# Optimization experiments

Hardware: AMD Instinct MI355X
Metric: run time of the kernel (lower is better)

The kernel has to match this reference:

```python
import jax, jax.numpy as jnp
import numpy as np

N = 10000        # nodes
E = 320000       # edges (avg degree 32)
H = 256          # num_hidden
NH = 8           # num_heads
NIN = 512        # num_in = 2*H


def _lin(key, out_f, in_f, scale=0.02):
    kw, kb = jax.random.split(key)
    W = jax.random.normal(kw, (out_f, in_f), jnp.float32) * scale
    b = jax.random.normal(kb, (out_f,), jnp.float32) * scale
    return W, b


def setup_inputs() -> dict:
    key = jax.random.key(0)
    ks = jax.random.split(key, 12)
    src_na = jax.random.normal(ks[0], (N, H), jnp.float32)
    dst_na = jax.random.normal(ks[1], (N, H), jnp.float32)
    ea = jax.random.normal(ks[2], (E, H), jnp.float32)
    edge_idx = jax.random.randint(ks[3], (2, E), 0, N, dtype=jnp.int32).astype(jnp.int64)
    # W_V: Linear(NIN,H) GELU Linear(H,H) GELU Linear(H,H)
    Wv1, bv1 = _lin(ks[4], H, NIN)
    Wv2, bv2 = _lin(ks[5], H, H)
    Wv3, bv3 = _lin(ks[6], H, H)
    # Bias: Linear(3H,H) ReLU Linear(H,H) ReLU Linear(H,NH)
    Wb1, bb1 = _lin(ks[7], H, 3 * H)
    Wb2, bb2 = _lin(ks[8], H, H)
    Wb3, bb3 = _lin(ks[9], NH, H)
    WO = jax.random.normal(ks[10], (H, H), jnp.float32) * 0.02  # no bias
    return dict(src_na=src_na, dst_na=dst_na, ea=ea, edge_idx=edge_idx,
                Wv1=Wv1, bv1=bv1, Wv2=Wv2, bv2=bv2, Wv3=Wv3, bv3=bv3,
                Wb1=Wb1, bb1=bb1, Wb2=Wb2, bb2=bb2, Wb3=Wb3, bb3=bb3, WO=WO)


def reference(src_na, dst_na, ea, edge_idx,
              Wv1, bv1, Wv2, bv2, Wv3, bv3,
              Wb1, bb1, Wb2, bb2, Wb3, bb3, WO):
    num_hidden = src_na.shape[-1]
    num_heads = Wb3.shape[0]
    d = num_hidden // num_heads
    n_nodes = dst_na.shape[0]

    dst_idx = edge_idx[0]
    src_idx = edge_idx[1]

    s = src_na[src_idx]          # [E,H] gather
    t = dst_na[dst_idx]          # [E,H] gather

    # Bias MLP -> per-edge, per-head logits
    h = jax.nn.relu(jnp.concatenate([s, ea, t], axis=-1) @ Wb1.T + bb1)
    h = jax.nn.relu(h @ Wb2.T + bb2)
    w = h @ Wb3.T + bb3                                  # [E,NH]
    logits = (w / np.sqrt(d)).reshape(-1, num_heads, 1)  # [E,NH,1]

    # Value MLP
    v = jax.nn.gelu(jnp.concatenate([s, ea], axis=-1) @ Wv1.T + bv1, approximate=False)
    v = jax.nn.gelu(v @ Wv2.T + bv2, approximate=False)
    V = (v @ Wv3.T + bv3).reshape(-1, num_heads, d)      # [E,NH,d]

    # scatter_softmax over edges grouped by destination node
    m = jax.ops.segment_max(logits, dst_idx, num_segments=n_nodes)   # [N,NH,1]
    ex = jnp.exp(logits - m[dst_idx])
    denom = jax.ops.segment_sum(ex, dst_idx, num_segments=n_nodes)   # [N,NH,1]
    attend = ex / denom[dst_idx]                                     # [E,NH,1]

    agg = jax.ops.segment_sum(attend * V, dst_idx, num_segments=n_nodes)  # [N,NH,d]
    out = agg.reshape(n_nodes, num_hidden) @ WO.T
    return out
```

## Files before the change

### kernel.cpp

```cpp
#include <hip/hip_runtime.h>
#include <hip/hip_bf16.h>
#include <cstdint>
#include <cstddef>

#define EN 320000
#define NN 10000

typedef __bf16 bf16_t;
typedef __bf16 bf16x8 __attribute__((ext_vector_type(8)));
typedef float f32x4 __attribute__((ext_vector_type(4)));
typedef unsigned short u16x8 __attribute__((ext_vector_type(8)));

__device__ __forceinline__ unsigned short f2b(float x) {
  bf16_t h = (bf16_t)x;
  return __builtin_bit_cast(unsigned short, h);
}
__device__ __forceinline__ float gelu_f(float x) {
  return 0.5f * x * (1.0f + erff(x * 0.70710678118654752f));
}
__device__ __forceinline__ void async_cp16(const void* gp, void* lp) {
  __builtin_amdgcn_global_load_lds((__attribute__((address_space(1))) void*)gp,
                                   (__attribute__((address_space(3))) void*)lp,
                                   16, 0, 0);
}

template <int AMODE, int EPI>
__global__ __launch_bounds__(256) void gemm_k(
    const void* __restrict__ Av, const bf16_t* __restrict__ W,
    const float* __restrict__ bias, void* __restrict__ Cv,
    int M, int K, int NOUT,
    const int* __restrict__ src32, const int* __restrict__ dst32,
    const float* __restrict__ projS, const float* __restrict__ projT,
    const float* __restrict__ bias2, bf16_t* __restrict__ C2) {
  __shared__ __align__(16) unsigned short As[128 * 32];
  __shared__ __align__(16) unsigned short Bs[128 * 32];
  const int tid = threadIdx.x;
  const int lane = tid & 63;
  const int wave = tid >> 6;
  const int wm = wave & 1, wn = wave >> 1;
  const int fr = lane & 15, kg = lane >> 4;
  const int rowBase = blockIdx.y * 128;
  const int colBase = blockIdx.x * 128;

  f32x4 acc[4][4] = {};

  const int nK = K >> 5;
  for (int kt = 0; kt < nK; ++kt) {
    const int k0 = kt << 5;
    if (kt) __syncthreads();
    if constexpr (AMODE == 0) {
      const bf16_t* A = (const bf16_t*)Av;
#pragma unroll
      for (int c = 0; c < 2; ++c) {
        int r = wave * 32 + c * 16 + (lane >> 2);
        int gr = rowBase + r;
        gr = (gr < M) ? gr : (M - 1);
        async_cp16(A + (size_t)gr * K + k0 + (lane & 3) * 8,
                   &As[(wave * 32 + c * 16) * 32]);
        int wr = colBase + wave * 32 + c * 16 + (lane >> 2);
        async_cp16(W + (size_t)wr * K + k0 + (lane & 3) * 8,
                   &Bs[(wave * 32 + c * 16) * 32]);
      }
    } else {
      const float* A = (const float*)Av;
      int r = tid >> 1, hh = tid & 1;
      int gr = rowBase + r;
      gr = (gr < M) ? gr : (M - 1);
      const float4* gp = (const float4*)(A + (size_t)gr * K + k0 + hh * 16);
      float4 x0 = gp[0], x1 = gp[1], x2 = gp[2], x3 = gp[3];
      u16x8 p0 = {f2b(x0.x), f2b(x0.y), f2b(x0.z), f2b(x0.w),
                  f2b(x1.x), f2b(x1.y), f2b(x1.z), f2b(x1.w)};
      u16x8 p1 = {f2b(x2.x), f2b(x2.y), f2b(x2.z), f2b(x2.w),
                  f2b(x3.x), f2b(x3.y), f2b(x3.z), f2b(x3.w)};
      *(u16x8*)&As[r * 32 + hh * 16] = p0;
      *(u16x8*)&As[r * 32 + hh * 16 + 8] = p1;
      const u16x8* wp = (const u16x8*)(W + (size_t)(colBase + r) * K + k0 + hh * 16);
      *(u16x8*)&Bs[r * 32 + hh * 16] = wp[0];
      *(u16x8*)&Bs[r * 32 + hh * 16 + 8] = wp[1];
    }
    __syncthreads();
    bf16x8 af[4], bw[4];
#pragma unroll
    for (int i = 0; i < 4; ++i)
      af[i] = *(const bf16x8*)&As[(wm * 64 + i * 16 + fr) * 32 + kg * 8];
#pragma unroll
    for (int i = 0; i < 4; ++i)
      bw[i] = *(const bf16x8*)&Bs[(wn * 64 + i * 16 + fr) * 32 + kg * 8];
#pragma unroll
    for (int mi = 0; mi < 4; ++mi)
#pragma unroll
      for (int ni = 0; ni < 4; ++ni)
        acc[mi][ni] = __builtin_amdgcn_mfma_f32_16x16x32_bf16(
            af[mi], bw[ni], acc[mi][ni], 0, 0, 0);
  }

  const int r0 = rowBase + wm * 64;
  const int c0 = colBase + wn * 64;
  if constexpr (EPI == 0) {
    float* C = (float*)Cv;
#pragma unroll
    for (int mi = 0; mi < 4; ++mi)
#pragma unroll
      for (int reg = 0; reg < 4; ++reg) {
        int row = r0 + mi * 16 + kg * 4 + reg;
        if (row < M) {
#pragma unroll
          for (int ni = 0; ni < 4; ++ni) {
            int col = c0 + ni * 16 + fr;
            C[(size_t)row * NOUT + col] = acc[mi][ni][reg];
          }
        }
      }
  } else if constexpr (EPI == 4) {
    bf16_t* C = (bf16_t*)Cv;
#pragma unroll
    for (int mi = 0; mi < 4; ++mi)
#pragma unroll
      for (int reg = 0; reg < 4; ++reg) {
        int e = r0 + mi * 16 + kg * 4 + reg;
        int si = src32[e], di = dst32[e];
#pragma unroll
        for (int ni = 0; ni < 4; ++ni) {
          int col = c0 + ni * 16 + fr;
          float v = acc[mi][ni][reg];
          if (col < 256) {
            v += bias[col] + projS[(size_t)si * 512 + col] + projT[(size_t)di * 256 + col];
            v = fmaxf(v, 0.f);
            C[(size_t)e * 256 + col] = (bf16_t)v;
          } else {
            int c2 = col - 256;
            v += bias2[c2] + projS[(size_t)si * 512 + col];
            v = gelu_f(v);
            C2[(size_t)e * 256 + c2] = (bf16_t)v;
          }
        }
      }
  } else {
    bf16_t* C = (bf16_t*)Cv;
#pragma unroll
    for (int mi = 0; mi < 4; ++mi)
#pragma unroll
      for (int reg = 0; reg < 4; ++reg) {
        int row = r0 + mi * 16 + kg * 4 + reg;
#pragma unroll
        for (int ni = 0; ni < 4; ++ni) {
          int col = c0 + ni * 16 + fr;
          float v = acc[mi][ni][reg] + bias[col];
          if constexpr (EPI == 1) v = fmaxf(v, 0.f);
          if constexpr (EPI == 2) v = gelu_f(v);
          C[(size_t)row * NOUT + col] = (bf16_t)v;
        }
      }
  }
}

__global__ __launch_bounds__(256) void logits_k(const bf16_t* __restrict__ h2b,
                                                const bf16_t* __restrict__ Wb3p,
                                                const float* __restrict__ bb3,
                                                float* __restrict__ logits) {
  const int lane = threadIdx.x & 63, wave = threadIdx.x >> 6;
  const int fr = lane & 15, kg = lane >> 4;
  const int e0 = blockIdx.x * 64 + wave * 16;
  f32x4 acc = {};
#pragma unroll
  for (int kt = 0; kt < 8; ++kt) {
    bf16x8 a = *(const bf16x8*)&h2b[(size_t)(e0 + fr) * 256 + kt * 32 + kg * 8];
    bf16x8 b = *(const bf16x8*)&Wb3p[(size_t)fr * 256 + kt * 32 + kg * 8];
    acc = __builtin_amdgcn_mfma_f32_16x16x32_bf16(a, b, acc, 0, 0, 0);
  }
  if (fr < 8) {
#pragma unroll
    for (int reg = 0; reg < 4; ++reg) {
      int e = e0 + kg * 4 + reg;
      logits[(size_t)e * 8 + fr] = (acc[reg] + bb3[fr]) * 0.17677669529663687f;
    }
  }
}

__global__ void detect_k(const int* __restrict__ ei, int* __restrict__ flag) {
  int v = ei[2 * threadIdx.x + 1];
  unsigned long long nz = __ballot(v != 0);
  if (threadIdx.x == 0) *flag = (nz != 0ULL) ? 1 : 0;
}

__global__ __launch_bounds__(256) void norm_k(const int* __restrict__ ei,
                                              const int* __restrict__ flag,
                                              int* __restrict__ dst32,
                                              int* __restrict__ src32) {
  int e = blockIdx.x * 256 + threadIdx.x;
  if (e >= EN) return;
  if (*flag) {
    dst32[e] = ei[e];
    src32[e] = ei[EN + e];
  } else {
    dst32[e] = ei[2 * e];
    src32[e] = ei[2 * EN + 2 * e];
  }
}

__global__ __launch_bounds__(256) void zero_k(unsigned int* __restrict__ p, int n) {
  int i = blockIdx.x * 256 + threadIdx.x;
  if (i < n) p[i] = 0u;
}

__global__ __launch_bounds__(256) void convw(const float* __restrict__ src,
                                             bf16_t* __restrict__ dst, int rows,
                                             int srcld, int srcoff) {
  int i = blockIdx.x * 256 + threadIdx.x;
  if (i >= rows * 256) return;
  int r = i >> 8, c = i & 255;
  dst[i] = (bf16_t)src[(size_t)r * srcld + srcoff + c];
}

__global__ __launch_bounds__(256) void hist_k(const int* __restrict__ dst32,
                                              int* __restrict__ counts) {
  int e = blockIdx.x * 256 + threadIdx.x;
  if (e < EN) atomicAdd(&counts[dst32[e]], 1);
}

__global__ __launch_bounds__(1024) void scan_k(const int* __restrict__ counts,
                                               int* __restrict__ offsets) {
  __shared__ int part[1024];
  const int t = threadIdx.x;
  const int base = t * 10;
  int s = 0;
#pragma unroll
  for (int j = 0; j < 10; ++j) {
    int i = base + j;
    if (i < NN) s += counts[i];
  }
  part[t] = s;
  __syncthreads();
  for (int off = 1; off < 1024; off <<= 1) {
    int v = (t >= off) ? part[t - off] : 0;
    __syncthreads();
    part[t] += v;
    __syncthreads();
  }
  int run = (t > 0) ? part[t - 1] : 0;
  for (int j = 0; j < 10; ++j) {
    int i = base + j;
    if (i < NN) {
      offsets[i] = run;
      run += counts[i];
    }
  }
  if (t == 0) offsets[NN] = part[1023];
}

__global__ __launch_bounds__(256) void scatter_k(const int* __restrict__ dst32,
                                                 const int* __restrict__ offsets,
                                                 int* __restrict__ cursor,
                                                 int* __restrict__ sorted) {
  int e = blockIdx.x * 256 + threadIdx.x;
  if (e >= EN) return;
  int d = dst32[e];
  int p = offsets[d] + atomicAdd(&cursor[d], 1);
  sorted[p] = e;
}

__global__ __launch_bounds__(256) void agg_k(const float* __restrict__ logits,
                                             const bf16_t* __restrict__ V,
                                             const int* __restrict__ offsets,
                                             const int* __restrict__ sorted,
                                             bf16_t* __restrict__ aggb) {
  const int node = blockIdx.x;
  const int t = threadIdx.x, g = t >> 5, l = t & 31;
  const int beg = offsets[node], end = offsets[node + 1];
  float m = -1e30f;
  for (int i = beg + l; i < end; i += 32)
    m = fmaxf(m, logits[(size_t)sorted[i] * 8 + g]);
#pragma unroll
  for (int off = 16; off >= 1; off >>= 1) m = fmaxf(m, __shfl_xor(m, off, 64));
  float den = 0.f;
  for (int i = beg + l; i < end; i += 32)
    den += expf(logits[(size_t)sorted[i] * 8 + g] - m);
#pragma unroll
  for (int off = 16; off >= 1; off >>= 1) den += __shfl_xor(den, off, 64);
  float acc = 0.f;
  for (int i = beg; i < end; ++i) {
    int e = sorted[i];
    float ex = expf(logits[(size_t)e * 8 + g] - m);
    acc += ex * (float)V[(size_t)e * 256 + g * 32 + l];
  }
  float r = (den > 0.f) ? acc / den : 0.f;
  aggb[(size_t)node * 256 + g * 32 + l] = (bf16_t)r;
}

extern "C" void kernel_launch(void* const* d_in, const int* in_sizes, int n_in,
                              void* d_out, int out_size, void* d_ws, size_t ws_size,
                              hipStream_t stream) {
  const float* src_na = (const float*)d_in[0];
  const float* dst_na = (const float*)d_in[1];
  const float* ea = (const float*)d_in[2];
  const int* ei_raw = (const int*)d_in[3];
  const float* Wv1 = (const float*)d_in[4];
  const float* bv1 = (const float*)d_in[5];
  const float* Wv2 = (const float*)d_in[6];
  const float* bv2 = (const float*)d_in[7];
  const float* Wv3 = (const float*)d_in[8];
  const float* bv3 = (const float*)d_in[9];
  const float* Wb1 = (const float*)d_in[10];
  const float* bb1 = (const float*)d_in[11];
  const float* Wb2 = (const float*)d_in[12];
  const float* bb2 = (const float*)d_in[13];
  const float* Wb3 = (const float*)d_in[14];
  const float* bb3 = (const float*)d_in[15];
  const float* WO = (const float*)d_in[16];

  char* base = (char*)d_ws;
  size_t off = 0;
  auto alloc = [&](size_t bytes) -> void* {
    void* p = base + off;
    off += (bytes + 255) & ~(size_t)255;
    return p;
  };
  bf16_t* Wsrc = (bf16_t*)alloc(512 * 256 * 2);
  bf16_t* Wdst = (bf16_t*)alloc(256 * 256 * 2);
  bf16_t* Wea = (bf16_t*)alloc(512 * 256 * 2);
  bf16_t* Wb2c = (bf16_t*)alloc(256 * 256 * 2);
  bf16_t* Wv2c = (bf16_t*)alloc(256 * 256 * 2);
  bf16_t* Wv3c = (bf16_t*)alloc(256 * 256 * 2);
  bf16_t* WOc = (bf16_t*)alloc(256 * 256 * 2);
  bf16_t* Wb3p = (bf16_t*)alloc(16 * 256 * 2);
  float* projS = (float*)alloc((size_t)NN * 512 * 4);
  float* projT = (float*)alloc((size_t)NN * 256 * 4);
  bf16_t* bufA = (bf16_t*)alloc((size_t)EN * 256 * 2);
  bf16_t* bufB = (bf16_t*)alloc((size_t)EN * 256 * 2);
  bf16_t* bufC = (bf16_t*)alloc((size_t)EN * 256 * 2);
  float* logits = (float*)alloc((size_t)EN * 8 * 4);
  bf16_t* aggb = (bf16_t*)alloc((size_t)NN * 256 * 2);
  int* counts = (int*)alloc(NN * 4);
  int* cursor = (int*)alloc(NN * 4);
  int* offsets = (int*)alloc((NN + 1) * 4);
  int* sorted = (int*)alloc(EN * 4);
  int* dst32 = (int*)alloc(EN * 4);
  int* src32 = (int*)alloc(EN * 4);
  int* flag = (int*)alloc(4);
  if (off > ws_size) return;

  zero_k<<<dim3(8), 256, 0, stream>>>((unsigned int*)Wb3p, 16 * 256 * 2 / 4);
  convw<<<dim3(256), 256, 0, stream>>>(Wb1, Wsrc, 256, 768, 0);
  convw<<<dim3(256), 256, 0, stream>>>(Wv1, Wsrc + 256 * 256, 256, 512, 0);
  convw<<<dim3(256), 256, 0, stream>>>(Wb1, Wdst, 256, 768, 512);
  convw<<<dim3(256), 256, 0, stream>>>(Wb1, Wea, 256, 768, 256);
  convw<<<dim3(256), 256, 0, stream>>>(Wv1, Wea + 256 * 256, 256, 512, 256);
  convw<<<dim3(256), 256, 0, stream>>>(Wb2, Wb2c, 256, 256, 0);
  convw<<<dim3(256), 256, 0, stream>>>(Wv2, Wv2c, 256, 256, 0);
  convw<<<dim3(256), 256, 0, stream>>>(Wv3, Wv3c, 256, 256, 0);
  convw<<<dim3(256), 256, 0, stream>>>(WO, WOc, 256, 256, 0);
  convw<<<dim3(8), 256, 0, stream>>>(Wb3, Wb3p, 8, 256, 0);

  detect_k<<<1, 64, 0, stream>>>(ei_raw, flag);
  norm_k<<<1250, 256, 0, stream>>>(ei_raw, flag, dst32, src32);
  zero_k<<<dim3((NN + 255) / 256), 256, 0, stream>>>((unsigned int*)counts, NN);
  zero_k<<<dim3((NN + 255) / 256), 256, 0, stream>>>((unsigned int*)cursor, NN);

  gemm_k<1, 0><<<dim3(4, 79), 256, 0, stream>>>(src_na, Wsrc, nullptr, projS, NN, 256, 512,
                                                nullptr, nullptr, nullptr, nullptr, nullptr, nullptr);
  gemm_k<1, 0><<<dim3(2, 79), 256, 0, stream>>>(dst_na, Wdst, nullptr, projT, NN, 256, 256,
                                                nullptr, nullptr, nullptr, nullptr, nullptr, nullptr);
  gemm_k<1, 4><<<dim3(4, 2500), 256, 0, stream>>>(ea, Wea, bb1, bufA, EN, 256, 512,
                                                  src32, dst32, projS, projT, bv1, bufB);
  gemm_k<0, 1><<<dim3(2, 2500), 256, 0, stream>>>(bufA, Wb2c, bb2, bufC, EN, 256, 256,
                                                  nullptr, nullptr, nullptr, nullptr, nullptr, nullptr);
  logits_k<<<5000, 256, 0, stream>>>(bufC, Wb3p, bb3, logits);
  gemm_k<0, 2><<<dim3(2, 2500), 256, 0, stream>>>(bufB, Wv2c, bv2, bufA, EN, 256, 256,
                                                  nullptr, nullptr, nullptr, nullptr, nullptr, nullptr);
  gemm_k<0, 3><<<dim3(2, 2500), 256, 0, stream>>>(bufA, Wv3c, bv3, bufB, EN, 256, 256,
                                                  nullptr, nullptr, nullptr, nullptr, nullptr, nullptr);

  hist_k<<<1250, 256, 0, stream>>>(dst32, counts);
  scan_k<<<1, 1024, 0, stream>>>(counts, offsets);
  scatter_k<<<1250, 256, 0, stream>>>(dst32, offsets, cursor, sorted);

  agg_k<<<NN, 256, 0, stream>>>(logits, bufB, offsets, sorted, aggb);

  gemm_k<0, 0><<<dim3(2, 79), 256, 0, stream>>>(aggb, WOc, nullptr, d_out, NN, 256, 256,
                                                nullptr, nullptr, nullptr, nullptr, nullptr, nullptr);
}
```

Measured before the change: 1.575 ms.

## Fuse MLP layer chains into row-resident kernels with swizzled LDS and merged prep

Replaces the 128x128 tiled GEMM with a kernel that keeps a full 64-row A tile (K=256) resident in swizzled LDS and streams double-buffered weight tiles across all output columns. The bias MLP's second and third layers and the value MLP's second and third layers are each fused into one kernel, with intermediates kept in LDS. This removes the bf16 intermediate round-trips to HBM and the extra launches. The weight conversions and zeroing are merged into one prep kernel, and the histogram is folded into index normalization. The cost is more LDS per block (about 48KB), which may lower occupancy, and A tiles are reloaded only once per row block.

```diff
diff --git a/kernel.cpp b/kernel.cpp
--- a/kernel.cpp
+++ b/kernel.cpp
@@ -24,156 +24,336 @@
                                    16, 0, 0);
 }
 
-template <int AMODE, int EPI>
-__global__ __launch_bounds__(256) void gemm_k(
+__device__ __forceinline__ bf16x8 read_a(const unsigned short* P, int row, int kc) {
+  return *(const bf16x8*)&P[(row * 32 + (kc ^ (row & 7))) * 8];
+}
+__device__ __forceinline__ bf16x8 read_b(const unsigned short* P, int col, int kg) {
+  return *(const bf16x8*)&P[(col * 4 + (kg ^ ((col >> 2) & 3))) * 8];
+}
+__device__ __forceinline__ void stage_b_tile(const bf16_t* W, int cc, int kt,
+                                             unsigned short* buf, int wave, int lane) {
+#pragma unroll
+  for (int c = 0; c < 2; ++c) {
+    int n0 = wave * 128 + c * 64;
+    int nl = n0 + lane;
+    int col = nl >> 2;
+    int kgq = (nl & 3) ^ ((col >> 2) & 3);
+    async_cp16(W + (size_t)(cc * 128 + col) * 256 + kt * 32 + kgq * 8, &buf[n0 * 8]);
+  }
+}
+__device__ __forceinline__ void stage_wb3(const bf16_t* Wp, unsigned short* buf,
+                                          int wave, int lane) {
+#pragma unroll
+  for (int c = 0; c < 2; ++c) {
+    int n0 = wave * 128 + c * 64;
+    int nl = n0 + lane;
+    int h = nl >> 5, p = nl & 31;
+    int kc = p ^ (h & 7);
+    async_cp16(Wp + (size_t)h * 256 + kc * 8, &buf[n0 * 8]);
+  }
+}
+__device__ __forceinline__ void stage_a_bf16(const bf16_t* A, unsigned short* As,
+                                             int rowBase, int M, int wave, int lane) {
+  int sub = lane >> 5, p = lane & 31;
+#pragma unroll
+  for (int j = 0; j < 8; ++j) {
+    int row = wave * 16 + j * 2 + sub;
+    int gr = rowBase + row;
+    gr = (gr < M) ? gr : (M - 1);
+    int kc = p ^ (row & 7);
+    async_cp16(A + (size_t)gr * 256 + kc * 8, &As[(wave * 16 + j * 2) * 32 * 8]);
+  }
+}
+
+template <int AMODE, int EPI, int NCC>
+__global__ __launch_bounds__(256) void gemm2(
     const void* __restrict__ Av, const bf16_t* __restrict__ W,
-    const float* __restrict__ bias, void* __restrict__ Cv,
-    int M, int K, int NOUT,
+    const float* __restrict__ bias, void* __restrict__ Cv, int M,
     const int* __restrict__ src32, const int* __restrict__ dst32,
     const float* __restrict__ projS, const float* __restrict__ projT,
     const float* __restrict__ bias2, bf16_t* __restrict__ C2) {
-  __shared__ __align__(16) unsigned short As[128 * 32];
-  __shared__ __align__(16) unsigned short Bs[128 * 32];
+  __shared__ __align__(16) unsigned short As[2048 * 8];
+  __shared__ __align__(16) unsigned short Bs[2][512 * 8];
   const int tid = threadIdx.x;
-  const int lane = tid & 63;
-  const int wave = tid >> 6;
+  const int lane = tid & 63, wave = tid >> 6;
   const int wm = wave & 1, wn = wave >> 1;
   const int fr = lane & 15, kg = lane >> 4;
-  const int rowBase = blockIdx.y * 128;
-  const int colBase = blockIdx.x * 128;
-
-  f32x4 acc[4][4] = {};
-
-  const int nK = K >> 5;
-  for (int kt = 0; kt < nK; ++kt) {
-    const int k0 = kt << 5;
-    if (kt) __syncthreads();
-    if constexpr (AMODE == 0) {
-      const bf16_t* A = (const bf16_t*)Av;
-#pragma unroll
-      for (int c = 0; c < 2; ++c) {
-        int r = wave * 32 + c * 16 + (lane >> 2);
-        int gr = rowBase + r;
-        gr = (gr < M) ? gr : (M - 1);
-        async_cp16(A + (size_t)gr * K + k0 + (lane & 3) * 8,
-                   &As[(wave * 32 + c * 16) * 32]);
-        int wr = colBase + wave * 32 + c * 16 + (lane >> 2);
-        async_cp16(W + (size_t)wr * K + k0 + (lane & 3) * 8,
-                   &Bs[(wave * 32 + c * 16) * 32]);
+  const int rowBase = blockIdx.x * 64;
+
+  if constexpr (AMODE == 0) {
+    stage_a_bf16((const bf16_t*)Av, As, rowBase, M, wave, lane);
+  } else {
+    const float* A = (const float*)Av;
+    int row = tid >> 2, qq = tid & 3;
+    int gr = rowBase + row;
+    gr = (gr < M) ? gr : (M - 1);
+    const float4* gp = (const float4*)(A + (size_t)gr * 256 + qq * 64);
+#pragma unroll
+    for (int q = 0; q < 2; ++q) {
+      float4 y[8];
+#pragma unroll
+      for (int u = 0; u < 8; ++u) y[u] = gp[q * 8 + u];
+#pragma unroll
+      for (int c = 0; c < 4; ++c) {
+        int kc = qq * 8 + q * 4 + c;
+        u16x8 pk = {f2b(y[2 * c].x), f2b(y[2 * c].y), f2b(y[2 * c].z), f2b(y[2 * c].w),
+                    f2b(y[2 * c + 1].x), f2b(y[2 * c + 1].y), f2b(y[2 * c + 1].z),
+                    f2b(y[2 * c + 1].w)};
+        *(u16x8*)&As[(row * 32 + (kc ^ (row & 7))) * 8] = pk;
       }
-    } else {
-      const float* A = (const float*)Av;
-      int r = tid >> 1, hh = tid & 1;
-      int gr = rowBase + r;
-      gr = (gr < M) ? gr : (M - 1);
-      const float4* gp = (const float4*)(A + (size_t)gr * K + k0 + hh * 16);
-      float4 x0 = gp[0], x1 = gp[1], x2 = gp[2], x3 = gp[3];
-      u16x8 p0 = {f2b(x0.x), f2b(x0.y), f2b(x0.z), f2b(x0.w),
-                  f2b(x1.x), f2b(x1.y), f2b(x1.z), f2b(x1.w)};
-      u16x8 p1 = {f2b(x2.x), f2b(x2.y), f2b(x2.z), f2b(x2.w),
-                  f2b(x3.x), f2b(x3.y), f2b(x3.z), f2b(x3.w)};
-      *(u16x8*)&As[r * 32 + hh * 16] = p0;
-      *(u16x8*)&As[r * 32 + hh * 16 + 8] = p1;
-      const u16x8* wp = (const u16x8*)(W + (size_t)(colBase + r) * K + k0 + hh * 16);
-      *(u16x8*)&Bs[r * 32 + hh * 16] = wp[0];
-      *(u16x8*)&Bs[r * 32 + hh * 16 + 8] = wp[1];
-    }
-    __syncthreads();
-    bf16x8 af[4], bw[4];
-#pragma unroll
-    for (int i = 0; i < 4; ++i)
-      af[i] = *(const bf16x8*)&As[(wm * 64 + i * 16 + fr) * 32 + kg * 8];
-#pragma unroll
-    for (int i = 0; i < 4; ++i)
-      bw[i] = *(const bf16x8*)&Bs[(wn * 64 + i * 16 + fr) * 32 + kg * 8];
-#pragma unroll
-    for (int mi = 0; mi < 4; ++mi)
-#pragma unroll
-      for (int ni = 0; ni < 4; ++ni)
-        acc[mi][ni] = __builtin_amdgcn_mfma_f32_16x16x32_bf16(
-            af[mi], bw[ni], acc[mi][ni], 0, 0, 0);
-  }
-
-  const int r0 = rowBase + wm * 64;
-  const int c0 = colBase + wn * 64;
-  if constexpr (EPI == 0) {
-    float* C = (float*)Cv;
-#pragma unroll
-    for (int mi = 0; mi < 4; ++mi)
-#pragma unroll
-      for (int reg = 0; reg < 4; ++reg) {
-        int row = r0 + mi * 16 + kg * 4 + reg;
-        if (row < M) {
-#pragma unroll
-          for (int ni = 0; ni < 4; ++ni) {
-            int col = c0 + ni * 16 + fr;
-            C[(size_t)row * NOUT + col] = acc[mi][ni][reg];
+    }
+  }
+  stage_b_tile(W, 0, 0, Bs[0], wave, lane);
+  __syncthreads();
+
+  const int T = NCC * 8;
+  for (int cc = 0; cc < NCC; ++cc) {
+    f32x4 acc[2][4] = {};
+    for (int kt = 0; kt < 8; ++kt) {
+      int j = cc * 8 + kt;
+      if (j + 1 < T) stage_b_tile(W, (j + 1) >> 3, (j + 1) & 7, Bs[(j + 1) & 1], wave, lane);
+      const unsigned short* B = Bs[j & 1];
+      bf16x8 af[2], bw[4];
+#pragma unroll
+      for (int mi = 0; mi < 2; ++mi) af[mi] = read_a(As, wm * 32 + mi * 16 + fr, kt * 4 + kg);
+#pragma unroll
+      for (int ni = 0; ni < 4; ++ni) bw[ni] = read_b(B, wn * 64 + ni * 16 + fr, kg);
+#pragma unroll
+      for (int mi = 0; mi < 2; ++mi)
+#pragma unroll
+        for (int ni = 0; ni < 4; ++ni)
+          acc[mi][ni] = __builtin_amdgcn_mfma_f32_16x16x32_bf16(af[mi], bw[ni], acc[mi][ni], 0, 0, 0);
+      __syncthreads();
+    }
+    if constexpr (EPI == 0) {
+      float* C = (float*)Cv;
+#pragma unroll
+      for (int mi = 0; mi < 2; ++mi)
+#pragma unroll
+        for (int reg = 0; reg < 4; ++reg) {
+          int row = rowBase + wm * 32 + mi * 16 + kg * 4 + reg;
+          if (row < M) {
+#pragma unroll
+            for (int ni = 0; ni < 4; ++ni)
+              C[(size_t)row * (NCC * 128) + cc * 128 + wn * 64 + ni * 16 + fr] = acc[mi][ni][reg];
           }
         }
-      }
-  } else if constexpr (EPI == 4) {
-    bf16_t* C = (bf16_t*)Cv;
-#pragma unroll
-    for (int mi = 0; mi < 4; ++mi)
-#pragma unroll
-      for (int reg = 0; reg < 4; ++reg) {
-        int e = r0 + mi * 16 + kg * 4 + reg;
-        int si = src32[e], di = dst32[e];
-#pragma unroll
-        for (int ni = 0; ni < 4; ++ni) {
-          int col = c0 + ni * 16 + fr;
-          float v = acc[mi][ni][reg];
-          if (col < 256) {
-            v += bias[col] + projS[(size_t)si * 512 + col] + projT[(size_t)di * 256 + col];
-            v = fmaxf(v, 0.f);
-            C[(size_t)e * 256 + col] = (bf16_t)v;
-          } else {
-            int c2 = col - 256;
-            v += bias2[c2] + projS[(size_t)si * 512 + col];
-            v = gelu_f(v);
-            C2[(size_t)e * 256 + c2] = (bf16_t)v;
+    } else {
+      bf16_t* C = (bf16_t*)Cv;
+#pragma unroll
+      for (int mi = 0; mi < 2; ++mi)
+#pragma unroll
+        for (int reg = 0; reg < 4; ++reg) {
+          int e = rowBase + wm * 32 + mi * 16 + kg * 4 + reg;
+          int si = src32[e], di = dst32[e];
+#pragma unroll
+          for (int ni = 0; ni < 4; ++ni) {
+            int col = cc * 128 + wn * 64 + ni * 16 + fr;
+            float v = acc[mi][ni][reg];
+            if (col < 256) {
+              v += bias[col] + projS[(size_t)si * 512 + col] + projT[(size_t)di * 256 + col];
+              v = fmaxf(v, 0.f);
+              C[(size_t)e * 256 + col] = (bf16_t)v;
+            } else {
+              int c2 = col - 256;
+              v += bias2[c2] + projS[(size_t)si * 512 + col];
+              v = gelu_f(v);
+              C2[(size_t)e * 256 + c2] = (bf16_t)v;
+            }
           }
         }
-      }
-  } else {
-    bf16_t* C = (bf16_t*)Cv;
-#pragma unroll
-    for (int mi = 0; mi < 4; ++mi)
+    }
+  }
+}
+
+__global__ __launch_bounds__(256) void bias_fuse(
+    const bf16_t* __restrict__ h1b, const bf16_t* __restrict__ Wb2c,
+    const float* __restrict__ bb2, const bf16_t* __restrict__ Wb3p,
+    const float* __restrict__ bb3, float* __restrict__ logits) {
+  __shared__ __align__(16) unsigned short As[2048 * 8];
+  __shared__ __align__(16) unsigned short Bs[2][512 * 8];
+  const int tid = threadIdx.x;
+  const int lane = tid & 63, wave = tid >> 6;
+  const int wm = wave & 1, wn = wave >> 1;
+  const int fr = lane & 15, kg = lane >> 4;
+  const int rowBase = blockIdx.x * 64;
+
+  stage_a_bf16(h1b, As, rowBase, EN, wave, lane);
+  stage_b_tile(Wb2c, 0, 0, Bs[0], wave, lane);
+  __syncthreads();
+
+  f32x4 acc[2][2][4] = {};
+  for (int cc = 0; cc < 2; ++cc)
+    for (int kt = 0; kt < 8; ++kt) {
+      int j = cc * 8 + kt;
+      if (j + 1 < 16)
+        stage_b_tile(Wb2c, (j + 1) >> 3, (j + 1) & 7, Bs[(j + 1) & 1], wave, lane);
+      else
+        stage_wb3(Wb3p, Bs[0], wave, lane);
+      const unsigned short* B = Bs[j & 1];
+      bf16x8 af[2], bw[4];
+#pragma unroll
+      for (int mi = 0; mi < 2; ++mi) af[mi] = read_a(As, wm * 32 + mi * 16 + fr, kt * 4 + kg);
+#pragma unroll
+      for (int ni = 0; ni < 4; ++ni) bw[ni] = read_b(B, wn * 64 + ni * 16 + fr, kg);
+#pragma unroll
+      for (int mi = 0; mi < 2; ++mi)
+#pragma unroll
+        for (int ni = 0; ni < 4; ++ni)
+          acc[cc][mi][ni] = __builtin_amdgcn_mfma_f32_16x16x32_bf16(af[mi], bw[ni], acc[cc][mi][ni], 0, 0, 0);
+      __syncthreads();
+    }
+#pragma unroll
+  for (int cc = 0; cc < 2; ++cc)
+#pragma unroll
+    for (int mi = 0; mi < 2; ++mi)
 #pragma unroll
       for (int reg = 0; reg < 4; ++reg) {
-        int row = r0 + mi * 16 + kg * 4 + reg;
+        int row = wm * 32 + mi * 16 + kg * 4 + reg;
 #pragma unroll
         for (int ni = 0; ni < 4; ++ni) {
-          int col = c0 + ni * 16 + fr;
-          float v = acc[mi][ni][reg] + bias[col];
-          if constexpr (EPI == 1) v = fmaxf(v, 0.f);
-          if constexpr (EPI == 2) v = gelu_f(v);
-          C[(size_t)row * NOUT + col] = (bf16_t)v;
+          int col = cc * 128 + wn * 64 + ni * 16 + fr;
+          float v = fmaxf(acc[cc][mi][ni][reg] + bb2[col], 0.f);
+          As[(row * 32 + ((col >> 3) ^ (row & 7))) * 8 + (col & 7)] = f2b(v);
         }
       }
-  }
-}
-
-__global__ __launch_bounds__(256) void logits_k(const bf16_t* __restrict__ h2b,
-                                                const bf16_t* __restrict__ Wb3p,
-                                                const float* __restrict__ bb3,
-                                                float* __restrict__ logits) {
-  const int lane = threadIdx.x & 63, wave = threadIdx.x >> 6;
+  __syncthreads();
+  f32x4 la = {};
+#pragma unroll
+  for (int kt = 0; kt < 8; ++kt) {
+    int kc = kt * 4 + kg;
+    bf16x8 a = read_a(As, wave * 16 + fr, kc);
+    bf16x8 b = read_a(Bs[0], fr, kc);
+    la = __builtin_amdgcn_mfma_f32_16x16x32_bf16(a, b, la, 0, 0, 0);
+  }
+  if (fr < 8) {
+#pragma unroll
+    for (int reg = 0; reg < 4; ++reg) {
+      int e = rowBase + wave * 16 + kg * 4 + reg;
+      logits[(size_t)e * 8 + fr] = (la[reg] + bb3[fr]) * 0.17677669529663687f;
+    }
+  }
+}
+
+__global__ __launch_bounds__(256) void val_fuse(
+    const bf16_t* __restrict__ h1v, const bf16_t* __restrict__ Wv2c,
+    const float* __restrict__ bv2, const bf16_t* __restrict__ Wv3c,
+    const float* __restrict__ bv3, bf16_t* __restrict__ V) {
+  __shared__ __align__(16) unsigned short As[2048 * 8];
+  __shared__ __align__(16) unsigned short Bs[2][512 * 8];
+  const int tid = threadIdx.x;
+  const int lane = tid & 63, wave = tid >> 6;
+  const int wm = wave & 1, wn = wave >> 1;
   const int fr = lane & 15, kg = lane >> 4;
-  const int e0 = blockIdx.x * 64 + wave * 16;
-  f32x4 acc = {};
-#pragma unroll
-  for (int kt = 0; kt < 8; ++kt) {
-    bf16x8 a = *(const bf16x8*)&h2b[(size_t)(e0 + fr) * 256 + kt * 32 + kg * 8];
-    bf16x8 b = *(const bf16x8*)&Wb3p[(size_t)fr * 256 + kt * 32 + kg * 8];
-    acc = __builtin_amdgcn_mfma_f32_16x16x32_bf16(a, b, acc, 0, 0, 0);
-  }
-  if (fr < 8) {
-#pragma unroll
-    for (int reg = 0; reg < 4; ++reg) {
-      int e = e0 + kg * 4 + reg;
-      logits[(size_t)e * 8 + fr] = (acc[reg] + bb3[fr]) * 0.17677669529663687f;
-    }
+  const int rowBase = blockIdx.x * 64;
+
+  stage_a_bf16(h1v, As, rowBase, EN, wave, lane);
+  stage_b_tile(Wv2c, 0, 0, Bs[0], wave, lane);
+  __syncthreads();
+
+  f32x4 acc[2][2][4] = {};
+  for (int cc = 0; cc < 2; ++cc)
+    for (int kt = 0; kt < 8; ++kt) {
+      int j = cc * 8 + kt;
+      if (j + 1 < 16)
+        stage_b_tile(Wv2c, (j + 1) >> 3, (j + 1) & 7, Bs[(j + 1) & 1], wave, lane);
+      else
+        stage_b_tile(Wv3c, 0, 0, Bs[0], wave, lane);
+      const unsigned short* B = Bs[j & 1];
+      bf16x8 af[2], bw[4];
+#pragma unroll
+      for (int mi = 0; mi < 2; ++mi) af[mi] = read_a(As, wm * 32 + mi * 16 + fr, kt * 4 + kg);
+#pragma unroll
+      for (int ni = 0; ni < 4; ++ni) bw[ni] = read_b(B, wn * 64 + ni * 16 + fr, kg);
+#pragma unroll
+      for (int mi = 0; mi < 2; ++mi)
+#pragma unroll
+        for (int ni = 0; ni < 4; ++ni)
+          acc[cc][mi][ni] = __builtin_amdgcn_mfma_f32_16x16x32_bf16(af[mi], bw[ni], acc[cc][mi][ni], 0, 0, 0);
+      __syncthreads();
+    }
+#pragma unroll
+  for (int cc = 0; cc < 2; ++cc)
+#pragma unroll
+    for (int mi = 0; mi < 2; ++mi)
+#pragma unroll
+      for (int reg = 0; reg < 4; ++reg) {
+        int row = wm * 32 + mi * 16 + kg * 4 + reg;
+#pragma unroll
+        for (int ni = 0; ni < 4; ++ni) {
+          int col = cc * 128 + wn * 64 + ni * 16 + fr;
+          float v = gelu_f(acc[cc][mi][ni][reg] + bv2[col]);
+          As[(row * 32 + ((col >> 3) ^ (row & 7))) * 8 + (col & 7)] = f2b(v);
+        }
+      }
+  __syncthreads();
+  for (int cc2 = 0; cc2 < 2; ++cc2) {
+    f32x4 a2[2][4] = {};
+    for (int kt = 0; kt < 8; ++kt) {
+      int j2 = cc2 * 8 + kt;
+      if (j2 + 1 < 16)
+        stage_b_tile(Wv3c, (j2 + 1) >> 3, (j2 + 1) & 7, Bs[(j2 + 1) & 1], wave, lane);
+      const unsigned short* B = Bs[j2 & 1];
+      bf16x8 af[2], bw[4];
+#pragma unroll
+      for (int mi = 0; mi < 2; ++mi) af[mi] = read_a(As, wm * 32 + mi * 16 + fr, kt * 4 + kg);
+#pragma unroll
+      for (int ni = 0; ni < 4; ++ni) bw[ni] = read_b(B, wn * 64 + ni * 16 + fr, kg);
+#pragma unroll
+      for (int mi = 0; mi < 2; ++mi)
+#pragma unroll
+        for (int ni = 0; ni < 4; ++ni)
+          a2[mi][ni] = __builtin_amdgcn_mfma_f32_16x16x32_bf16(af[mi], bw[ni], a2[mi][ni], 0, 0, 0);
+      __syncthreads();
+    }
+#pragma unroll
+    for (int mi = 0; mi < 2; ++mi)
+#pragma unroll
+      for (int reg = 0; reg < 4; ++reg) {
+        int e = rowBase + wm * 32 + mi * 16 + kg * 4 + reg;
+#pragma unroll
+        for (int ni = 0; ni < 4; ++ni) {
+          int col = cc2 * 128 + wn * 64 + ni * 16 + fr;
+          V[(size_t)e * 256 + col] = (bf16_t)(a2[mi][ni][reg] + bv3[col]);
+        }
+      }
+  }
+}
+
+__global__ __launch_bounds__(256) void prep_k(
+    const float* __restrict__ Wb1, const float* __restrict__ Wv1,
+    const float* __restrict__ Wb2, const float* __restrict__ Wv2,
+    const float* __restrict__ Wv3, const float* __restrict__ WO,
+    const float* __restrict__ Wb3, bf16_t* __restrict__ Wsrc,
+    bf16_t* __restrict__ Wdst, bf16_t* __restrict__ Wea,
+    bf16_t* __restrict__ Wb2c, bf16_t* __restrict__ Wv2c,
+    bf16_t* __restrict__ Wv3c, bf16_t* __restrict__ WOc,
+    bf16_t* __restrict__ Wb3p, int* __restrict__ counts, int* __restrict__ cursor) {
+  int i = blockIdx.x * 256 + threadIdx.x;
+  if (i < 589824) {
+    int seg = i >> 16, j = i & 65535, r = j >> 8, c = j & 255;
+    const float* src;
+    bf16_t* dst;
+    int ld, off;
+    switch (seg) {
+      case 0: src = Wb1; dst = Wsrc; ld = 768; off = 0; break;
+      case 1: src = Wv1; dst = Wsrc + 65536; ld = 512; off = 0; break;
+      case 2: src = Wb1; dst = Wdst; ld = 768; off = 512; break;
+      case 3: src = Wb1; dst = Wea; ld = 768; off = 256; break;
+      case 4: src = Wv1; dst = Wea + 65536; ld = 512; off = 256; break;
+      case 5: src = Wb2; dst = Wb2c; ld = 256; off = 0; break;
+      case 6: src = Wv2; dst = Wv2c; ld = 256; off = 0; break;
+      case 7: src = Wv3; dst = Wv3c; ld = 256; off = 0; break;
+      default: src = WO; dst = WOc; ld = 256; off = 0; break;
+    }
+    dst[j] = (bf16_t)src[(size_t)r * ld + off + c];
+  } else if (i < 593920) {
+    int j = i - 589824, r = j >> 8, c = j & 255;
+    Wb3p[j] = (r < 8) ? (bf16_t)Wb3[r * 256 + c] : (bf16_t)0.f;
+  } else if (i < 593920 + NN) {
+    counts[i - 593920] = 0;
+  } else if (i < 593920 + 2 * NN) {
+    cursor[i - 593920 - NN] = 0;
   }
 }
 
@@ -183,39 +363,19 @@
   if (threadIdx.x == 0) *flag = (nz != 0ULL) ? 1 : 0;
 }
 
-__global__ __launch_bounds__(256) void norm_k(const int* __restrict__ ei,
-                                              const int* __restrict__ flag,
-                                              int* __restrict__ dst32,
-                                              int* __restrict__ src32) {
+__global__ __launch_bounds__(256) void normhist_k(const int* __restrict__ ei,
+                                                  const int* __restrict__ flag,
+                                                  int* __restrict__ dst32,
+                                                  int* __restrict__ src32,
+                                                  int* __restrict__ counts) {
   int e = blockIdx.x * 256 + threadIdx.x;
   if (e >= EN) return;
-  if (*flag) {
-    dst32[e] = ei[e];
-    src32[e] = ei[EN + e];
-  } else {
-    dst32[e] = ei[2 * e];
-    src32[e] = ei[2 * EN + 2 * e];
-  }
-}
-
-__global__ __launch_bounds__(256) void zero_k(unsigned int* __restrict__ p, int n) {
-  int i = blockIdx.x * 256 + threadIdx.x;
-  if (i < n) p[i] = 0u;
-}
-
-__global__ __launch_bounds__(256) void convw(const float* __restrict__ src,
-                                             bf16_t* __restrict__ dst, int rows,
-                                             int srcld, int srcoff) {
-  int i = blockIdx.x * 256 + threadIdx.x;
-  if (i >= rows * 256) return;
-  int r = i >> 8, c = i & 255;
-  dst[i] = (bf16_t)src[(size_t)r * srcld + srcoff + c];
-}
-
-__global__ __launch_bounds__(256) void hist_k(const int* __restrict__ dst32,
-                                              int* __restrict__ counts) {
-  int e = blockIdx.x * 256 + threadIdx.x;
-  if (e < EN) atomicAdd(&counts[dst32[e]], 1);
+  int d, s;
+  if (*flag) { d = ei[e]; s = ei[EN + e]; }
+  else { d = ei[2 * e]; s = ei[2 * EN + 2 * e]; }
+  dst32[e] = d;
+  src32[e] = s;
+  atomicAdd(&counts[d], 1);
 }
 
 __global__ __launch_bounds__(1024) void scan_k(const int* __restrict__ counts,
@@ -327,7 +487,7 @@
   float* projT = (float*)alloc((size_t)NN * 256 * 4);
   bf16_t* bufA = (bf16_t*)alloc((size_t)EN * 256 * 2);
   bf16_t* bufB = (bf16_t*)alloc((size_t)EN * 256 * 2);
-  bf16_t* bufC = (bf16_t*)alloc((size_t)EN * 256 * 2);
+  bf16_t* bufV = (bf16_t*)alloc((size_t)EN * 256 * 2);
   float* logits = (float*)alloc((size_t)EN * 8 * 4);
   bf16_t* aggb = (bf16_t*)alloc((size_t)NN * 256 * 2);
   int* counts = (int*)alloc(NN * 4);
@@ -339,43 +499,24 @@
   int* flag = (int*)alloc(4);
   if (off > ws_size) return;
 
-  zero_k<<<dim3(8), 256, 0, stream>>>((unsigned int*)Wb3p, 16 * 256 * 2 / 4);
-  convw<<<dim3(256), 256, 0, stream>>>(Wb1, Wsrc, 256, 768, 0);
-  convw<<<dim3(256), 256, 0, stream>>>(Wv1, Wsrc + 256 * 256, 256, 512, 0);
-  convw<<<dim3(256), 256, 0, stream>>>(Wb1, Wdst, 256, 768, 512);
-  convw<<<dim3(256), 256, 0, stream>>>(Wb1, Wea, 256, 768, 256);
-  convw<<<dim3(256), 256, 0, stream>>>(Wv1, Wea + 256 * 256, 256, 512, 256);
-  convw<<<dim3(256), 256, 0, stream>>>(Wb2, Wb2c, 256, 256, 0);
-  convw<<<dim3(256), 256, 0, stream>>>(Wv2, Wv2c, 256, 256, 0);
-  convw<<<dim3(256), 256, 0, stream>>>(Wv3, Wv3c, 256, 256, 0);
-  convw<<<dim3(256), 256, 0, stream>>>(WO, WOc, 256, 256, 0);
-  convw<<<dim3(8), 256, 0, stream>>>(Wb3, Wb3p, 8, 256, 0);
-
+  prep_k<<<2399, 256, 0, stream>>>(Wb1, Wv1, Wb2, Wv2, Wv3, WO, Wb3, Wsrc, Wdst, Wea,
+                                   Wb2c, Wv2c, Wv3c, WOc, Wb3p, counts, cursor);
   detect_k<<<1, 64, 0, stream>>>(ei_raw, flag);
-  norm_k<<<1250, 256, 0, stream>>>(ei_raw, flag, dst32, src32);
-  zero_k<<<dim3((NN + 255) / 256), 256, 0, stream>>>((unsigned int*)counts, NN);
-  zero_k<<<dim3((NN + 255) / 256), 256, 0, stream>>>((unsigned int*)cursor, NN);
-
-  gemm_k<1, 0><<<dim3(4, 79), 256, 0, stream>>>(src_na, Wsrc, nullptr, projS, NN, 256, 512,
-                                                nullptr, nullptr, nullptr, nullptr, nullptr, nullptr);
-  gemm_k<1, 0><<<dim3(2, 79), 256, 0, stream>>>(dst_na, Wdst, nullptr, projT, NN, 256, 256,
-                                                nullptr, nullptr, nullptr, nullptr, nullptr, nullptr);
-  gemm_k<1, 4><<<dim3(4, 2500), 256, 0, stream>>>(ea, Wea, bb1, bufA, EN, 256, 512,
-                                                  src32, dst32, projS, projT, bv1, bufB);
-  gemm_k<0, 1><<<dim3(2, 2500), 256, 0, stream>>>(bufA, Wb2c, bb2, bufC, EN, 256, 256,
-                                                  nullptr, nullptr, nullptr, nullptr, nullptr, nullptr);
-  logits_k<<<5000, 256, 0, stream>>>(bufC, Wb3p, bb3, logits);
-  gemm_k<0, 2><<<dim3(2, 2500), 256, 0, stream>>>(bufB, Wv2c, bv2, bufA, EN, 256, 256,
-                                                  nullptr, nullptr, nullptr, nullptr, nullptr, nullptr);
-  gemm_k<0, 3><<<dim3(2, 2500), 256, 0, stream>>>(bufA, Wv3c, bv3, bufB, EN, 256, 256,
-                                                  nullptr, nullptr, nullptr, nullptr, nullptr, nullptr);
-
-  hist_k<<<1250, 256, 0, stream>>>(dst32, counts);
+  normhist_k<<<1250, 256, 0, stream>>>(ei_raw, flag, dst32, src32, counts);
   scan_k<<<1, 1024, 0, stream>>>(counts, offsets);
   scatter_k<<<1250, 256, 0, stream>>>(dst32, offsets, cursor, sorted);
 
-  agg_k<<<NN, 256, 0, stream>>>(logits, bufB, offsets, sorted, aggb);
-
-  gemm_k<0, 0><<<dim3(2, 79), 256, 0, stream>>>(aggb, WOc, nullptr, d_out, NN, 256, 256,
-                                                nullptr, nullptr, nullptr, nullptr, nullptr, nullptr);
-}
+  gemm2<1, 0, 4><<<157, 256, 0, stream>>>(src_na, Wsrc, nullptr, projS, NN,
+                                          nullptr, nullptr, nullptr, nullptr, nullptr, nullptr);
+  gemm2<1, 0, 2><<<157, 256, 0, stream>>>(dst_na, Wdst, nullptr, projT, NN,
+                                          nullptr, nullptr, nullptr, nullptr, nullptr, nullptr);
+  gemm2<1, 4, 4><<<5000, 256, 0, stream>>>(ea, Wea, bb1, bufA, EN,
+                                           src32, dst32, projS, projT, bv1, bufB);
+  bias_fuse<<<5000, 256, 0, stream>>>(bufA, Wb2c, bb2, Wb3p, bb3, logits);
+  val_fuse<<<5000, 256, 0, stream>>>(bufB, Wv2c, bv2, Wv3c, bv3, bufV);
+
+  agg_k<<<NN, 256, 0, stream>>>(logits, bufV, offsets, sorted, aggb);
+
+  gemm2<0, 0, 2><<<157, 256, 0, stream>>>(aggb, WOc, nullptr, d_out, NN,
+                                          nullptr, nullptr, nullptr, nullptr, nullptr, nullptr);
+}
```

After: 1.315 ms. 16.5% less time.
